# Kernel optimization log

Hardware: AMD Instinct MI355X
Metric: run time of the kernel (lower is better)

The kernel has to match this reference:

```python
import jax, jax.numpy as jnp
import numpy as np

H = 8
D = 512
DK = D // H
B = 16
N = 8192


def setup_inputs() -> dict:
    key = jax.random.key(0)
    k1, k2, k3, k4 = jax.random.split(key, 4)
    x = jax.random.normal(k1, (B, N, D), dtype=jnp.float32)
    W_k = jax.random.normal(k2, (D, D), dtype=jnp.float32) * (1.0 / np.sqrt(D))
    W_g = jax.random.normal(k3, (D, D), dtype=jnp.float32) * (1.0 / np.sqrt(D))
    query = jax.random.normal(k4, (H, 1, DK), dtype=jnp.float32)
    return {"x": x, "W_k": W_k, "W_g": W_g, "query": query}


def reference(x, W_k, W_g, query):
    b, n, d = x.shape
    # nn.Linear: y = x @ W.T  (no bias)
    K = (x @ W_k.T).reshape(b, n, H, DK).transpose(0, 2, 1, 3)  # (b,h,n,dk)
    G = (x @ W_g.T).reshape(b, n, H, DK).transpose(0, 2, 1, 3)  # (b,h,n,dk)
    xh = x.reshape(b, n, H, DK).transpose(0, 2, 1, 3)           # (b,h,n,dk)
    gated = jnp.tanh(K) * jax.nn.sigmoid(G)                     # (b,h,n,dk)
    # single-query attention: scores (b,h,1,n)
    scores = jnp.einsum('hmd,bhnd->bhmn', query, gated)
    attn = jax.nn.softmax(scores, axis=-1)
    out = jnp.einsum('bhmn,bhnd->bhmd', attn, xh)               # (b,h,1,dk)
    out = out.transpose(0, 2, 1, 3).reshape(b, 1, H * DK)
    return out.squeeze()  # (b, d)
```

## Files before the change

kernel.cpp:

```cpp
#include <hip/hip_runtime.h>
#include <hip/hip_bf16.h>

#define H_ 8
#define D_ 512
#define DK_ 64
#define B_ 16
#define N_ 8192
#define M_ (B_ * N_)

typedef __attribute__((ext_vector_type(8))) short short8;
typedef __attribute__((ext_vector_type(4))) float floatx4;

__device__ __forceinline__ void glds16(const void* g, void* l) {
    __builtin_amdgcn_global_load_lds((const __attribute__((address_space(1))) void*)g,
                                     (__attribute__((address_space(3))) void*)l,
                                     16, 0, 0);
}

__device__ __forceinline__ unsigned short f2bf(float f) {
    unsigned u = __float_as_uint(f);
    return (unsigned short)((u + 0x7fffu + ((u >> 16) & 1u)) >> 16);
}

__global__ __launch_bounds__(256) void cvt_kernel(const float* __restrict__ src,
                                                  unsigned short* __restrict__ dst, int n4) {
    int i = blockIdx.x * blockDim.x + threadIdx.x;
    int stride = gridDim.x * blockDim.x;
    for (; i < n4; i += stride) {
        float4 v = ((const float4*)src)[i];
        ushort4 o;
        o.x = f2bf(v.x); o.y = f2bf(v.y); o.z = f2bf(v.z); o.w = f2bf(v.w);
        ((ushort4*)dst)[i] = o;
    }
}

__global__ __launch_bounds__(256, 2) void gemm_score_kernel(
    const unsigned short* __restrict__ xb,
    const unsigned short* __restrict__ wkb,
    const unsigned short* __restrict__ wgb,
    const float* __restrict__ query,
    float* __restrict__ s_buf)
{
    __shared__ unsigned short lds_a[128 * 32];
    __shared__ unsigned short lds_k[128 * 32];
    __shared__ unsigned short lds_g[128 * 32];

    const int t = threadIdx.x;
    const int lane = t & 63;
    const int wave = t >> 6;
    const int wm = wave >> 1, wn = wave & 1;
    const int jc = blockIdx.x * 128;
    const int m0 = blockIdx.y * 128;

    floatx4 acc_k[4][4], acc_g[4][4];
#pragma unroll
    for (int i = 0; i < 4; ++i)
#pragma unroll
        for (int j = 0; j < 4; ++j) { acc_k[i][j] = (floatx4)0.f; acc_g[i][j] = (floatx4)0.f; }

    const int r0 = t >> 2, c0 = t & 3;
    const int r1 = 64 + r0;
    const size_t xo0 = (size_t)(m0 + r0) * 512 + c0 * 8;
    const size_t xo1 = (size_t)(m0 + r1) * 512 + c0 * 8;
    const size_t wo0 = (size_t)(jc + r0) * 512 + c0 * 8;
    const size_t wo1 = (size_t)(jc + r1) * 512 + c0 * 8;
    unsigned short* la0 = lds_a + t * 8;
    unsigned short* la1 = lds_a + (256 + t) * 8;
    unsigned short* lk0 = lds_k + t * 8;
    unsigned short* lk1 = lds_k + (256 + t) * 8;
    unsigned short* lg0 = lds_g + t * 8;
    unsigned short* lg1 = lds_g + (256 + t) * 8;

    const int fr = lane & 15;
    const int fk = (lane >> 4) * 8;

    for (int k0 = 0; k0 < 512; k0 += 32) {
        glds16(xb + xo0 + k0, la0);
        glds16(xb + xo1 + k0, la1);
        glds16(wkb + wo0 + k0, lk0);
        glds16(wkb + wo1 + k0, lk1);
        glds16(wgb + wo0 + k0, lg0);
        glds16(wgb + wo1 + k0, lg1);
        __syncthreads();

        short8 a[4], bk[4], bg[4];
#pragma unroll
        for (int mi = 0; mi < 4; ++mi)
            a[mi] = *(const short8*)(lds_a + (wm * 64 + mi * 16 + fr) * 32 + fk);
#pragma unroll
        for (int ni = 0; ni < 4; ++ni) {
            bk[ni] = *(const short8*)(lds_k + (wn * 64 + ni * 16 + fr) * 32 + fk);
            bg[ni] = *(const short8*)(lds_g + (wn * 64 + ni * 16 + fr) * 32 + fk);
        }
#pragma unroll
        for (int mi = 0; mi < 4; ++mi)
#pragma unroll
            for (int ni = 0; ni < 4; ++ni) {
                acc_k[mi][ni] = __builtin_amdgcn_mfma_f32_16x16x32_bf16(a[mi], bk[ni], acc_k[mi][ni], 0, 0, 0);
                acc_g[mi][ni] = __builtin_amdgcn_mfma_f32_16x16x32_bf16(a[mi], bg[ni], acc_g[mi][ni], 0, 0, 0);
            }
        __syncthreads();
    }

    const int h = blockIdx.x * 2 + wn;
    float qv[4];
#pragma unroll
    for (int ni = 0; ni < 4; ++ni) qv[ni] = query[h * 64 + ni * 16 + fr];

#pragma unroll
    for (int mi = 0; mi < 4; ++mi) {
#pragma unroll
        for (int r = 0; r < 4; ++r) {
            float v = 0.f;
#pragma unroll
            for (int ni = 0; ni < 4; ++ni) {
                float kv = acc_k[mi][ni][r];
                float gv = acc_g[mi][ni][r];
                float e2k = __expf(2.f * kv);
                float th = 1.f - 2.f / (e2k + 1.f);
                float sg = 1.f / (1.f + __expf(-gv));
                v += qv[ni] * th * sg;
            }
            v += __shfl_xor(v, 1);
            v += __shfl_xor(v, 2);
            v += __shfl_xor(v, 4);
            v += __shfl_xor(v, 8);
            if (fr == 0) {
                int mg = m0 + wm * 64 + mi * 16 + (lane >> 4) * 4 + r;
                int b = mg >> 13, n = mg & 8191;
                s_buf[((size_t)(b * 8 + h) << 13) + n] = v;
            }
        }
    }
}

__global__ __launch_bounds__(256) void stats_kernel(const float* __restrict__ s_buf,
                                                    float* __restrict__ mb, float* __restrict__ lb) {
    const int bh = blockIdx.x;
    const float* s = s_buf + ((size_t)bh << 13);
    const int t = threadIdx.x;
    float mx = -3.0e38f;
    for (int i = t; i < 8192; i += 256) mx = fmaxf(mx, s[i]);
#pragma unroll
    for (int m = 32; m > 0; m >>= 1) mx = fmaxf(mx, __shfl_xor(mx, m));
    __shared__ float red[8];
    if ((t & 63) == 0) red[t >> 6] = mx;
    __syncthreads();
    mx = fmaxf(fmaxf(red[0], red[1]), fmaxf(red[2], red[3]));
    float sum = 0.f;
    for (int i = t; i < 8192; i += 256) sum += __expf(s[i] - mx);
#pragma unroll
    for (int m = 32; m > 0; m >>= 1) sum += __shfl_xor(sum, m);
    if ((t & 63) == 0) red[4 + (t >> 6)] = sum;
    __syncthreads();
    if (t == 0) { mb[bh] = mx; lb[bh] = red[4] + red[5] + red[6] + red[7]; }
}

__global__ __launch_bounds__(256) void out_kernel(
    const unsigned short* __restrict__ xb, const float* __restrict__ s_buf,
    const float* __restrict__ mb, const float* __restrict__ lb,
    float* __restrict__ out) {
    const int b = blockIdx.x >> 5;
    const int chunk = blockIdx.x & 31;
    const int n0 = chunk * 256;
    const int t = threadIdx.x;
    __shared__ float w[8 * 256];
    for (int i = t; i < 2048; i += 256) {
        int hh = i >> 8, nn = i & 255;
        int bh = b * 8 + hh;
        w[i] = __expf(s_buf[((size_t)bh << 13) + n0 + nn] - mb[bh]) / lb[bh];
    }
    __syncthreads();
    const int rg = t >> 6;
    const int d0 = (t & 63) * 8;
    const float* wh = w + ((d0 >> 6) << 8);
    float acc[8] = {0.f, 0.f, 0.f, 0.f, 0.f, 0.f, 0.f, 0.f};
    for (int nn = rg; nn < 256; nn += 4) {
        const uint4 u = *(const uint4*)(xb + (((size_t)(b * 8192 + n0 + nn)) << 9) + d0);
        float ww = wh[nn];
        acc[0] += ww * __uint_as_float(u.x << 16);
        acc[1] += ww * __uint_as_float(u.x & 0xffff0000u);
        acc[2] += ww * __uint_as_float(u.y << 16);
        acc[3] += ww * __uint_as_float(u.y & 0xffff0000u);
        acc[4] += ww * __uint_as_float(u.z << 16);
        acc[5] += ww * __uint_as_float(u.z & 0xffff0000u);
        acc[6] += ww * __uint_as_float(u.w << 16);
        acc[7] += ww * __uint_as_float(u.w & 0xffff0000u);
    }
#pragma unroll
    for (int j = 0; j < 8; ++j) atomicAdd(&out[b * 512 + d0 + j], acc[j]);
}

extern "C" void kernel_launch(void* const* d_in, const int* in_sizes, int n_in,
                              void* d_out, int out_size, void* d_ws, size_t ws_size,
                              hipStream_t stream) {
    const float* x  = (const float*)d_in[0];
    const float* Wk = (const float*)d_in[1];
    const float* Wg = (const float*)d_in[2];
    const float* q  = (const float*)d_in[3];
    float* out = (float*)d_out;

    char* ws = (char*)d_ws;
    unsigned short* xb  = (unsigned short*)ws;
    unsigned short* wkb = (unsigned short*)(ws + 134217728ull);
    unsigned short* wgb = (unsigned short*)(ws + 134742016ull);
    float* s_buf = (float*)(ws + 135266304ull);
    float* mb = (float*)(ws + 139460608ull);
    float* lb = (float*)(ws + 139461120ull);

    hipMemsetAsync(d_out, 0, 512 * B_ * sizeof(float), stream);

    hipLaunchKernelGGL(cvt_kernel, dim3(8192), dim3(256), 0, stream, x, xb, (B_ * N_ * D_) / 4);
    hipLaunchKernelGGL(cvt_kernel, dim3(256), dim3(256), 0, stream, Wk, wkb, (D_ * D_) / 4);
    hipLaunchKernelGGL(cvt_kernel, dim3(256), dim3(256), 0, stream, Wg, wgb, (D_ * D_) / 4);
    hipLaunchKernelGGL(gemm_score_kernel, dim3(4, 1024), dim3(256), 0, stream, xb, wkb, wgb, q, s_buf);
    hipLaunchKernelGGL(stats_kernel, dim3(128), dim3(256), 0, stream, s_buf, mb, lb);
    hipLaunchKernelGGL(out_kernel, dim3(512), dim3(256), 0, stream, xb, s_buf, mb, lb, out);
}
```

Baseline: 650.0 us.

## Drop x-to-bf16 conversion pass; load fp32 x into GEMM and convert in-register

Removes the separate full conversion of x to bf16. The GEMM now streams fp32 x tiles into LDS and packs them to bf16 right before the MFMA, and the output kernel reads fp32 x directly. XOR swizzles are added to the LDS layouts of both A and B to avoid bank conflicts. This saves a 256MB read plus a 128MB write pass. In exchange the GEMM reads twice the bytes for x across its 4 column blocks and uses more LDS, and the out kernel reads fp32 instead of bf16. Rounding also changes from round-to-nearest-even to round-half-up.

```diff
diff --git a/kernel.cpp b/kernel.cpp
--- a/kernel.cpp
+++ b/kernel.cpp
@@ -20,6 +20,11 @@
 __device__ __forceinline__ unsigned short f2bf(float f) {
     unsigned u = __float_as_uint(f);
     return (unsigned short)((u + 0x7fffu + ((u >> 16) & 1u)) >> 16);
+}
+
+__device__ __forceinline__ unsigned pack_bf2(float x, float y) {
+    return __builtin_amdgcn_perm(__float_as_uint(y) + 0x8000u,
+                                 __float_as_uint(x) + 0x8000u, 0x07060302u);
 }
 
 __global__ __launch_bounds__(256) void cvt_kernel(const float* __restrict__ src,
@@ -35,13 +40,13 @@
 }
 
 __global__ __launch_bounds__(256, 2) void gemm_score_kernel(
-    const unsigned short* __restrict__ xb,
+    const float* __restrict__ x,
     const unsigned short* __restrict__ wkb,
     const unsigned short* __restrict__ wgb,
     const float* __restrict__ query,
     float* __restrict__ s_buf)
 {
-    __shared__ unsigned short lds_a[128 * 32];
+    __shared__ float lds_a[128 * 32];
     __shared__ unsigned short lds_k[128 * 32];
     __shared__ unsigned short lds_g[128 * 32];
 
@@ -58,39 +63,61 @@
 #pragma unroll
         for (int j = 0; j < 4; ++j) { acc_k[i][j] = (floatx4)0.f; acc_g[i][j] = (floatx4)0.f; }
 
-    const int r0 = t >> 2, c0 = t & 3;
-    const int r1 = 64 + r0;
-    const size_t xo0 = (size_t)(m0 + r0) * 512 + c0 * 8;
-    const size_t xo1 = (size_t)(m0 + r1) * 512 + c0 * 8;
-    const size_t wo0 = (size_t)(jc + r0) * 512 + c0 * 8;
-    const size_t wo1 = (size_t)(jc + r1) * 512 + c0 * 8;
-    unsigned short* la0 = lds_a + t * 8;
-    unsigned short* la1 = lds_a + (256 + t) * 8;
-    unsigned short* lk0 = lds_k + t * 8;
-    unsigned short* lk1 = lds_k + (256 + t) * 8;
-    unsigned short* lg0 = lds_g + t * 8;
-    unsigned short* lg1 = lds_g + (256 + t) * 8;
+    int ar[4], ac[4];
+#pragma unroll
+    for (int i = 0; i < 4; ++i) {
+        int p = i * 256 + t;
+        int r = p >> 3;
+        ar[i] = r;
+        ac[i] = (p & 7) ^ (r & 7);
+    }
+    int br[2], bc[2];
+#pragma unroll
+    for (int i = 0; i < 2; ++i) {
+        int p = i * 256 + t;
+        int r = p >> 2;
+        br[i] = r;
+        bc[i] = (p & 3) ^ ((r >> 1) & 3);
+    }
 
     const int fr = lane & 15;
-    const int fk = (lane >> 4) * 8;
+    const int q  = lane >> 4;
+    const int sw_a0 = (2 * q) ^ (fr & 7);
+    const int sw_a1 = sw_a0 ^ 1;
+    const int sw_b  = q ^ ((fr >> 1) & 3);
 
     for (int k0 = 0; k0 < 512; k0 += 32) {
-        glds16(xb + xo0 + k0, la0);
-        glds16(xb + xo1 + k0, la1);
-        glds16(wkb + wo0 + k0, lk0);
-        glds16(wkb + wo1 + k0, lk1);
-        glds16(wgb + wo0 + k0, lg0);
-        glds16(wgb + wo1 + k0, lg1);
+#pragma unroll
+        for (int i = 0; i < 4; ++i)
+            glds16(x + (size_t)(m0 + ar[i]) * 512 + k0 + ac[i] * 4,
+                   lds_a + (size_t)(i * 256 + t) * 4);
+#pragma unroll
+        for (int i = 0; i < 2; ++i) {
+            glds16(wkb + (size_t)(jc + br[i]) * 512 + k0 + bc[i] * 8,
+                   lds_k + (size_t)(i * 256 + t) * 8);
+            glds16(wgb + (size_t)(jc + br[i]) * 512 + k0 + bc[i] * 8,
+                   lds_g + (size_t)(i * 256 + t) * 8);
+        }
         __syncthreads();
 
         short8 a[4], bk[4], bg[4];
 #pragma unroll
-        for (int mi = 0; mi < 4; ++mi)
-            a[mi] = *(const short8*)(lds_a + (wm * 64 + mi * 16 + fr) * 32 + fk);
+        for (int mi = 0; mi < 4; ++mi) {
+            int r = wm * 64 + mi * 16 + fr;
+            float4 f0 = *(const float4*)(lds_a + (r * 8 + sw_a0) * 4);
+            float4 f1 = *(const float4*)(lds_a + (r * 8 + sw_a1) * 4);
+            union { unsigned u[4]; short8 s; } tmp;
+            tmp.u[0] = pack_bf2(f0.x, f0.y);
+            tmp.u[1] = pack_bf2(f0.z, f0.w);
+            tmp.u[2] = pack_bf2(f1.x, f1.y);
+            tmp.u[3] = pack_bf2(f1.z, f1.w);
+            a[mi] = tmp.s;
+        }
 #pragma unroll
         for (int ni = 0; ni < 4; ++ni) {
-            bk[ni] = *(const short8*)(lds_k + (wn * 64 + ni * 16 + fr) * 32 + fk);
-            bg[ni] = *(const short8*)(lds_g + (wn * 64 + ni * 16 + fr) * 32 + fk);
+            int r = wn * 64 + ni * 16 + fr;
+            bk[ni] = *(const short8*)(lds_k + (r * 4 + sw_b) * 8);
+            bg[ni] = *(const short8*)(lds_g + (r * 4 + sw_b) * 8);
         }
 #pragma unroll
         for (int mi = 0; mi < 4; ++mi)
@@ -157,7 +184,7 @@
 }
 
 __global__ __launch_bounds__(256) void out_kernel(
-    const unsigned short* __restrict__ xb, const float* __restrict__ s_buf,
+    const float* __restrict__ x, const float* __restrict__ s_buf,
     const float* __restrict__ mb, const float* __restrict__ lb,
     float* __restrict__ out) {
     const int b = blockIdx.x >> 5;
@@ -176,16 +203,14 @@
     const float* wh = w + ((d0 >> 6) << 8);
     float acc[8] = {0.f, 0.f, 0.f, 0.f, 0.f, 0.f, 0.f, 0.f};
     for (int nn = rg; nn < 256; nn += 4) {
-        const uint4 u = *(const uint4*)(xb + (((size_t)(b * 8192 + n0 + nn)) << 9) + d0);
+        const float4* row = (const float4*)(x + (((size_t)(b * 8192 + n0 + nn)) << 9) + d0);
+        float4 v0 = row[0];
+        float4 v1 = row[1];
         float ww = wh[nn];
-        acc[0] += ww * __uint_as_float(u.x << 16);
-        acc[1] += ww * __uint_as_float(u.x & 0xffff0000u);
-        acc[2] += ww * __uint_as_float(u.y << 16);
-        acc[3] += ww * __uint_as_float(u.y & 0xffff0000u);
-        acc[4] += ww * __uint_as_float(u.z << 16);
-        acc[5] += ww * __uint_as_float(u.z & 0xffff0000u);
-        acc[6] += ww * __uint_as_float(u.w << 16);
-        acc[7] += ww * __uint_as_float(u.w & 0xffff0000u);
+        acc[0] += ww * v0.x; acc[1] += ww * v0.y;
+        acc[2] += ww * v0.z; acc[3] += ww * v0.w;
+        acc[4] += ww * v1.x; acc[5] += ww * v1.y;
+        acc[6] += ww * v1.z; acc[7] += ww * v1.w;
     }
 #pragma unroll
     for (int j = 0; j < 8; ++j) atomicAdd(&out[b * 512 + d0 + j], acc[j]);
@@ -201,19 +226,17 @@
     float* out = (float*)d_out;
 
     char* ws = (char*)d_ws;
-    unsigned short* xb  = (unsigned short*)ws;
-    unsigned short* wkb = (unsigned short*)(ws + 134217728ull);
-    unsigned short* wgb = (unsigned short*)(ws + 134742016ull);
-    float* s_buf = (float*)(ws + 135266304ull);
-    float* mb = (float*)(ws + 139460608ull);
-    float* lb = (float*)(ws + 139461120ull);
+    unsigned short* wkb = (unsigned short*)ws;
+    unsigned short* wgb = (unsigned short*)(ws + 524288ull);
+    float* s_buf = (float*)(ws + 1048576ull);
+    float* mb = (float*)(ws + 5242880ull);
+    float* lb = (float*)(ws + 5243392ull);
 
     hipMemsetAsync(d_out, 0, 512 * B_ * sizeof(float), stream);
 
-    hipLaunchKernelGGL(cvt_kernel, dim3(8192), dim3(256), 0, stream, x, xb, (B_ * N_ * D_) / 4);
     hipLaunchKernelGGL(cvt_kernel, dim3(256), dim3(256), 0, stream, Wk, wkb, (D_ * D_) / 4);
     hipLaunchKernelGGL(cvt_kernel, dim3(256), dim3(256), 0, stream, Wg, wgb, (D_ * D_) / 4);
-    hipLaunchKernelGGL(gemm_score_kernel, dim3(4, 1024), dim3(256), 0, stream, xb, wkb, wgb, q, s_buf);
+    hipLaunchKernelGGL(gemm_score_kernel, dim3(4, 1024), dim3(256), 0, stream, x, wkb, wgb, q, s_buf);
     hipLaunchKernelGGL(stats_kernel, dim3(128), dim3(256), 0, stream, s_buf, mb, lb);
-    hipLaunchKernelGGL(out_kernel, dim3(512), dim3(256), 0, stream, xb, s_buf, mb, lb, out);
-}
+    hipLaunchKernelGGL(out_kernel, dim3(512), dim3(256), 0, stream, x, s_buf, mb, lb, out);
+}
```

Result: faster. 630.7 us (-3.0%).
